# Optimization experiments

Hardware: AMD Instinct MI355X
Metric: run time of the kernel (lower is better)

The kernel has to match this reference:

```python
import jax, jax.numpy as jnp
import numpy as np

N = 100000      # nodes
D = 128         # per-component feature dim
E = 3200000     # edges (avg degree 32)
NUM_CLS = 40
EPS = 1e-7


def lorentz_logmap0(x):
    # Lorentz model, curvature -1, origin o = (1, 0, ..., 0).
    # log_o(x) = arccosh(x0) * (x - x0*o) / ||x - x0*o||  ; keeps full dim, time comp -> 0
    x0 = x[..., :1]
    u = jnp.concatenate([jnp.zeros_like(x0), x[..., 1:]], axis=-1)
    un = jnp.sqrt(jnp.clip(x0 * x0 - 1.0, EPS))
    return jnp.arccosh(jnp.maximum(x0, 1.0)) * u / un


def sphere_logmap0(x):
    # Unit sphere, origin o = (1, 0, ..., 0).
    # log_o(x) = arccos(<o,x>) * (x - <o,x> o) / ||x - <o,x> o||
    c = x[..., :1]
    u = jnp.concatenate([jnp.zeros_like(c), x[..., 1:]], axis=-1)
    un = jnp.sqrt(jnp.clip(1.0 - c * c, EPS))
    return jnp.arccos(jnp.clip(c, -1.0, 1.0)) * u / un


def setup_inputs() -> dict:
    key = jax.random.key(0)
    k1, k2, k3, k4, k5 = jax.random.split(key, 5)
    x_E = jax.random.normal(k1, (N, D), jnp.float32)
    # valid hyperboloid points: x0 = sqrt(1 + ||rest||^2)
    rest = 0.5 * jax.random.normal(k2, (N, D - 1), jnp.float32)
    x0 = jnp.sqrt(1.0 + jnp.sum(rest * rest, axis=-1, keepdims=True))
    x_H = jnp.concatenate([x0, rest], axis=-1)
    # valid sphere points: unit norm
    xs = jax.random.normal(k3, (N, D), jnp.float32)
    x_S = xs / jnp.linalg.norm(xs, axis=-1, keepdims=True)
    W = jax.random.normal(k4, (3 * D, NUM_CLS), jnp.float32) / np.sqrt(3 * D)
    edge_index = jax.random.randint(k5, (2, E), 0, N, dtype=jnp.int32)
    return {"x_E": x_E, "x_H": x_H, "x_S": x_S, "W": W, "edge_index": edge_index}


def reference(x_E, x_H, x_S, W, edge_index):
    # logmap0 projections + concat
    x = jnp.concatenate([x_E, lorentz_logmap0(x_H), sphere_logmap0(x_S)], axis=-1)  # [N, 3D]
    # GCNConv(bias=False): transform first (num_cls << in_dim), then normalized aggregation
    h = x @ W  # [N, C]
    row, col = edge_index[0], edge_index[1]
    loop = jnp.arange(N, dtype=edge_index.dtype)
    row = jnp.concatenate([row, loop])
    col = jnp.concatenate([col, loop])
    deg = jax.ops.segment_sum(jnp.ones_like(col, dtype=h.dtype), col, num_segments=N)
    dinv = jnp.where(deg > 0, jax.lax.rsqrt(jnp.maximum(deg, 1.0)), 0.0)
    norm = dinv[row] * dinv[col]  # [E+N]
    out = jax.ops.segment_sum(h[row] * norm[:, None], col, num_segments=N)  # [N, C]
    return out
```

## Files before the change

### kernel.cpp

```cpp
#include <hip/hip_runtime.h>
#include <math.h>

constexpr int NN   = 100000;
constexpr int DIM  = 128;
constexpr int NE   = 3200000;
constexpr int NCLS = 40;
constexpr float EPSF = 1e-7f;

constexpr int BSH  = 9;
constexpr int BSZ  = 1 << BSH;
constexpr int NBKT = (NN + BSZ - 1) >> BSH;
constexpr int CAP  = 18432;
constexpr int AEPB = 8192;
constexpr int ABLK = (NE + AEPB - 1) / AEPB;

constexpr int GSTR = 64;

typedef __attribute__((ext_vector_type(8))) short bf16x8;
typedef __attribute__((ext_vector_type(8))) unsigned short u16x8;
typedef __attribute__((ext_vector_type(4))) float f32x4;

__device__ __forceinline__ unsigned short f2bf(float f) {
    unsigned u = __builtin_bit_cast(unsigned, f);
    unsigned r = u + 0x7FFFu + ((u >> 16) & 1u);
    return (unsigned short)(r >> 16);
}
__device__ __forceinline__ float bf2f(unsigned short b) {
    return __builtin_bit_cast(float, (unsigned)b << 16);
}

__global__ __launch_bounds__(256) void binA_kernel(const int* __restrict__ row,
                                                   const int* __restrict__ col,
                                                   int* __restrict__ gcur,
                                                   unsigned* __restrict__ pairs) {
    __shared__ int hist[256];
    __shared__ int lofx[256];
    __shared__ int gbase[256];
    __shared__ unsigned sortedw[AEPB];
    __shared__ int dstg[AEPB];

    int t = threadIdx.x;
    int e0 = blockIdx.x * AEPB;
    int cnt = min(AEPB, NE - e0);

    hist[t] = 0;
    __syncthreads();
    for (int k = t; k < cnt; k += 256) atomicAdd(&hist[col[e0 + k] >> BSH], 1);
    __syncthreads();

    int h = hist[t];
    if (t < NBKT && h > 0) gbase[t] = atomicAdd(&gcur[t], h);
    lofx[t] = h;
    __syncthreads();
    for (int d = 1; d < 256; d <<= 1) {
        int o = (t >= d) ? lofx[t - d] : 0;
        __syncthreads();
        lofx[t] += o;
        __syncthreads();
    }
    int excl = lofx[t] - h;
    lofx[t] = excl;
    hist[t] = excl;
    __syncthreads();

    for (int k = t; k < cnt; k += 256) {
        int c = col[e0 + k], r = row[e0 + k];
        int b = c >> BSH;
        int pos = atomicAdd(&hist[b], 1);
        sortedw[pos] = ((unsigned)(c & (BSZ - 1)) << 17) | (unsigned)r;
        dstg[pos] = b * CAP + gbase[b] + (pos - lofx[b]);
    }
    __syncthreads();
    for (int k = t; k < cnt; k += 256) pairs[dstg[k]] = sortedw[k];
}

__global__ __launch_bounds__(1024) void dinv_kernel(const int* __restrict__ gcur,
                                                    const unsigned* __restrict__ pairs,
                                                    float* __restrict__ dinvt) {
    __shared__ int hist[BSZ];
    int t = threadIdx.x;
    int b = blockIdx.x;
    if (t < BSZ) hist[t] = 0;
    __syncthreads();
    int cnt = gcur[b];
    const unsigned* pb = pairs + (size_t)b * CAP;
    for (int i = t; i < cnt; i += 1024) atomicAdd(&hist[pb[i] >> 17], 1);
    __syncthreads();
    if (t < BSZ) {
        int n = (b << BSH) + t;
        if (n < NN) dinvt[n] = rsqrtf((float)(hist[t] + 1));
    }
}

__global__ __launch_bounds__(256) void wpack_kernel(const float* __restrict__ W,
                                                    unsigned short* __restrict__ wbf) {
    int idx = blockIdx.x * 256 + threadIdx.x;
    if (idx >= 12 * 3 * 2 * 64 * 8) return;
    int j    = idx & 7;
    int lane = (idx >> 3) & 63;
    int hl   = (idx >> 9) & 1;
    int rest = idx >> 10;
    int t    = rest % 3;
    int kc   = rest / 3;
    int k = kc * 32 + 8 * (lane >> 4) + j;
    int c = 16 * t + (lane & 15);
    float w = (c < NCLS) ? W[k * NCLS + c] : 0.f;
    unsigned short hi = f2bf(w);
    wbf[idx] = (hl == 0) ? hi : f2bf(w - bf2f(hi));
}

__global__ __launch_bounds__(256) void h_kernel(
    const float* __restrict__ xE, const float* __restrict__ xH,
    const float* __restrict__ xS, const unsigned short* __restrict__ wbf,
    const float* __restrict__ dinvt, unsigned short* __restrict__ gbf) {

    int t = threadIdx.x;
    int lane = t & 63;
    int wv = t >> 6;
    int n0 = blockIdx.x * 64;
    int r  = lane & 15;
    int kq = lane >> 4;
    int myrow = n0 + 16 * wv + r;
    bool rowok = myrow < NN;

    f32x4 acc0 = {0.f, 0.f, 0.f, 0.f};
    f32x4 acc1 = acc0, acc2 = acc0;

    const bf16x8* wfr = reinterpret_cast<const bf16x8*>(wbf);

    for (int m = 0; m < 3; ++m) {
        const float* xb = (m == 0) ? xE : (m == 1) ? xH : xS;
        const float* xrow = xb + (size_t)myrow * DIM;

        float4 xf[8];
#pragma unroll
        for (int kc4 = 0; kc4 < 4; ++kc4) {
            int off = kc4 * 32 + kq * 8;
            xf[2 * kc4]     = rowok ? *reinterpret_cast<const float4*>(xrow + off)
                                    : make_float4(0.f, 0.f, 0.f, 0.f);
            xf[2 * kc4 + 1] = rowok ? *reinterpret_cast<const float4*>(xrow + off + 4)
                                    : make_float4(0.f, 0.f, 0.f, 0.f);
        }

        float scm = 1.f;
        if (m > 0) {
            float x0 = rowok ? xrow[0] : 1.f;
            if (m == 1) {
                scm = acoshf(fmaxf(x0, 1.f)) * rsqrtf(fmaxf(x0 * x0 - 1.f, EPSF));
            } else {
                float cc = fminf(fmaxf(x0, -1.f), 1.f);
                scm = acosf(cc) * rsqrtf(fmaxf(1.f - x0 * x0, EPSF));
            }
        }

#pragma unroll
        for (int kc4 = 0; kc4 < 4; ++kc4) {
            float4 f0 = xf[2 * kc4], f1 = xf[2 * kc4 + 1];
            float a[8] = {f0.x, f0.y, f0.z, f0.w, f1.x, f1.y, f1.z, f1.w};
            if (m > 0 && kc4 == 0 && kq == 0) a[0] = 0.f;

            bf16x8 ah;
#pragma unroll
            for (int j = 0; j < 8; ++j)
                ah[j] = (short)f2bf(a[j] * scm);

            int kc = m * 4 + kc4;
            const bf16x8* wb = wfr + (size_t)(kc * 3) * 2 * 64;
            bf16x8 bh0 = wb[0 * 128 + 0 * 64 + lane];
            bf16x8 bl0 = wb[0 * 128 + 1 * 64 + lane];
            bf16x8 bh1 = wb[1 * 128 + 0 * 64 + lane];
            bf16x8 bl1 = wb[1 * 128 + 1 * 64 + lane];
            bf16x8 bh2 = wb[2 * 128 + 0 * 64 + lane];
            bf16x8 bl2 = wb[2 * 128 + 1 * 64 + lane];

            acc0 = __builtin_amdgcn_mfma_f32_16x16x32_bf16(ah, bh0, acc0, 0, 0, 0);
            acc0 = __builtin_amdgcn_mfma_f32_16x16x32_bf16(ah, bl0, acc0, 0, 0, 0);
            acc1 = __builtin_amdgcn_mfma_f32_16x16x32_bf16(ah, bh1, acc1, 0, 0, 0);
            acc1 = __builtin_amdgcn_mfma_f32_16x16x32_bf16(ah, bl1, acc1, 0, 0, 0);
            acc2 = __builtin_amdgcn_mfma_f32_16x16x32_bf16(ah, bh2, acc2, 0, 0, 0);
            acc2 = __builtin_amdgcn_mfma_f32_16x16x32_bf16(ah, bl2, acc2, 0, 0, 0);
        }
    }

    int nbase = n0 + 16 * wv + 4 * kq;
    float4 dv = make_float4(0.f, 0.f, 0.f, 0.f);
    if (nbase < NN)
        dv = *reinterpret_cast<const float4*>(dinvt + nbase);
    float dg[4] = {dv.x, dv.y, dv.z, dv.w};

#pragma unroll
    for (int i = 0; i < 4; ++i) {
        int n = nbase + i;
        if (n < NN) {
            float di = dg[i];
            unsigned short* gr = gbf + (size_t)n * GSTR;
            gr[r]      = f2bf(acc0[i] * di);
            gr[16 + r] = f2bf(acc1[i] * di);
            if (r < 8)
                gr[32 + r] = f2bf(acc2[i] * di);
        }
    }
}

__global__ __launch_bounds__(1024) void fusedBG_kernel(
    const int* __restrict__ gcur, const unsigned* __restrict__ pairs,
    const unsigned short* __restrict__ gbf, float* __restrict__ out) {

    __shared__ int srow[CAP];
    __shared__ int hist[512];
    __shared__ int sc[1024];

    int t = threadIdx.x;
    int b = blockIdx.x;
    int cnt = gcur[b];
    const unsigned* pb = pairs + (size_t)b * CAP;

    if (t < 512) hist[t] = 0;
    __syncthreads();
    for (int i = t; i < cnt; i += 1024) atomicAdd(&hist[pb[i] >> 17], 1);
    __syncthreads();

    int v = (t < 512) ? hist[t] : 0;
    sc[t] = v;
    __syncthreads();
    for (int d = 1; d < 1024; d <<= 1) {
        int o = (t >= d) ? sc[t - d] : 0;
        __syncthreads();
        sc[t] += o;
        __syncthreads();
    }
    int excl = sc[t] - v;
    __syncthreads();
    if (t < 512) { sc[t] = excl; hist[t] = excl; }
    __syncthreads();

    for (int i = t; i < cnt; i += 1024) {
        unsigned w = pb[i];
        int pos = atomicAdd(&hist[w >> 17], 1);
        srow[pos] = (int)(w & 0x1FFFFu);
    }
    __syncthreads();

    const u16x8* gball = reinterpret_cast<const u16x8*>(gbf);
    for (int task = t; task < BSZ * 5; task += 1024) {
        int c  = task / 5;
        int c8 = task - c * 5;
        int n = (b << BSH) + c;
        if (n >= NN) continue;
        int s = sc[c];
        int e = (c == BSZ - 1) ? cnt : sc[c + 1];
        float dinv = rsqrtf((float)(e - s + 1));

        const u16x8* gb = gball + c8;
        u16x8 sv = gb[(size_t)n * 8];
        float a0[8], a1[8], a2[8], a3[8];
#pragma unroll
        for (int k = 0; k < 8; ++k) {
            a0[k] = bf2f(sv[k]); a1[k] = 0.f; a2[k] = 0.f; a3[k] = 0.f;
        }

        int j = s;
        for (; j + 3 < e; j += 4) {
            int r0 = srow[j], r1 = srow[j + 1], r2 = srow[j + 2], r3 = srow[j + 3];
            u16x8 v0 = gb[(size_t)r0 * 8];
            u16x8 v1 = gb[(size_t)r1 * 8];
            u16x8 v2 = gb[(size_t)r2 * 8];
            u16x8 v3 = gb[(size_t)r3 * 8];
#pragma unroll
            for (int k = 0; k < 8; ++k) {
                a0[k] += bf2f(v0[k]); a1[k] += bf2f(v1[k]);
                a2[k] += bf2f(v2[k]); a3[k] += bf2f(v3[k]);
            }
        }
        for (; j < e; ++j) {
            u16x8 vv = gb[(size_t)srow[j] * 8];
#pragma unroll
            for (int k = 0; k < 8; ++k) a0[k] += bf2f(vv[k]);
        }

        float* on = out + (size_t)n * NCLS + c8 * 8;
        float4 o0, o1;
        o0.x = (a0[0] + a1[0] + a2[0] + a3[0]) * dinv;
        o0.y = (a0[1] + a1[1] + a2[1] + a3[1]) * dinv;
        o0.z = (a0[2] + a1[2] + a2[2] + a3[2]) * dinv;
        o0.w = (a0[3] + a1[3] + a2[3] + a3[3]) * dinv;
        o1.x = (a0[4] + a1[4] + a2[4] + a3[4]) * dinv;
        o1.y = (a0[5] + a1[5] + a2[5] + a3[5]) * dinv;
        o1.z = (a0[6] + a1[6] + a2[6] + a3[6]) * dinv;
        o1.w = (a0[7] + a1[7] + a2[7] + a3[7]) * dinv;
        *reinterpret_cast<float4*>(on)     = o0;
        *reinterpret_cast<float4*>(on + 4) = o1;
    }
}

extern "C" void kernel_launch(void* const* d_in, const int* in_sizes, int n_in,
                              void* d_out, int out_size, void* d_ws, size_t ws_size,
                              hipStream_t stream) {
    const float* xE = (const float*)d_in[0];
    const float* xH = (const float*)d_in[1];
    const float* xS = (const float*)d_in[2];
    const float* W  = (const float*)d_in[3];
    const int*   ei = (const int*)d_in[4];
    const int* row = ei;
    const int* col = ei + NE;
    float* out = (float*)d_out;

    auto pad = [](size_t x) { return (x + 255) & ~(size_t)255; };
    char* p = (char*)d_ws;
    int* gcur = (int*)p;                p += pad((size_t)NBKT * 4);
    unsigned* pairs = (unsigned*)p;     p += pad((size_t)NBKT * CAP * 4);
    unsigned short* gbf = (unsigned short*)p;
    p += pad((size_t)NN * GSTR * 2);
    float* dinvt = (float*)p;           p += pad((size_t)NN * 4);
    unsigned short* wbf = (unsigned short*)p;

    hipMemsetAsync(gcur, 0, (size_t)NBKT * 4, stream);

    wpack_kernel<<<(12 * 3 * 2 * 64 * 8 + 255) / 256, 256, 0, stream>>>(W, wbf);
    binA_kernel<<<ABLK, 256, 0, stream>>>(row, col, gcur, pairs);
    dinv_kernel<<<NBKT, 1024, 0, stream>>>(gcur, pairs, dinvt);
    h_kernel<<<(NN + 63) / 64, 256, 0, stream>>>(xE, xH, xS, wbf, dinvt, gbf);
    fusedBG_kernel<<<NBKT, 1024, 0, stream>>>(gcur, pairs, gbf, out);
}
```

Before: 143.9 us.

## Co-schedule edge binning and dense transform in one interleaved hybrid kernel

Merges the edge-binning kernel and the feature-transform (MFMA) kernel into a single launch where every third block bins edges and the other blocks compute unscaled h rows, so the memory-bound scatter and compute-bound GEMM can overlap on the GPU. The edges-per-bin-block count is halved so the block counts interleave. The dinv scaling moves into the degree kernel, which now rescales the bf16 h rows in place after computing degrees. The cost is an extra read-modify-write pass over gbf and a second bf16 rounding of h.

```diff
diff --git a/kernel.cpp b/kernel.cpp
--- a/kernel.cpp
+++ b/kernel.cpp
@@ -11,8 +11,9 @@
 constexpr int BSZ  = 1 << BSH;
 constexpr int NBKT = (NN + BSZ - 1) >> BSH;
 constexpr int CAP  = 18432;
-constexpr int AEPB = 8192;
+constexpr int AEPB = 4096;
 constexpr int ABLK = (NE + AEPB - 1) / AEPB;
+constexpr int HBLK = (NN + 63) / 64 + 1;
 
 constexpr int GSTR = 64;
 
@@ -29,54 +30,145 @@
     return __builtin_bit_cast(float, (unsigned)b << 16);
 }
 
-__global__ __launch_bounds__(256) void binA_kernel(const int* __restrict__ row,
-                                                   const int* __restrict__ col,
-                                                   int* __restrict__ gcur,
-                                                   unsigned* __restrict__ pairs) {
+__global__ __launch_bounds__(256) void hybrid_kernel(
+    const int* __restrict__ row, const int* __restrict__ col,
+    int* __restrict__ gcur, unsigned* __restrict__ pairs,
+    const float* __restrict__ xE, const float* __restrict__ xH,
+    const float* __restrict__ xS, const unsigned short* __restrict__ wbf,
+    unsigned short* __restrict__ gbf) {
+
     __shared__ int hist[256];
     __shared__ int lofx[256];
     __shared__ int gbase[256];
     __shared__ unsigned sortedw[AEPB];
     __shared__ int dstg[AEPB];
 
+    int bid = blockIdx.x;
     int t = threadIdx.x;
-    int e0 = blockIdx.x * AEPB;
-    int cnt = min(AEPB, NE - e0);
-
-    hist[t] = 0;
-    __syncthreads();
-    for (int k = t; k < cnt; k += 256) atomicAdd(&hist[col[e0 + k] >> BSH], 1);
-    __syncthreads();
-
-    int h = hist[t];
-    if (t < NBKT && h > 0) gbase[t] = atomicAdd(&gcur[t], h);
-    lofx[t] = h;
-    __syncthreads();
-    for (int d = 1; d < 256; d <<= 1) {
-        int o = (t >= d) ? lofx[t - d] : 0;
-        __syncthreads();
-        lofx[t] += o;
-        __syncthreads();
-    }
-    int excl = lofx[t] - h;
-    lofx[t] = excl;
-    hist[t] = excl;
-    __syncthreads();
-
-    for (int k = t; k < cnt; k += 256) {
-        int c = col[e0 + k], r = row[e0 + k];
-        int b = c >> BSH;
-        int pos = atomicAdd(&hist[b], 1);
-        sortedw[pos] = ((unsigned)(c & (BSZ - 1)) << 17) | (unsigned)r;
-        dstg[pos] = b * CAP + gbase[b] + (pos - lofx[b]);
-    }
-    __syncthreads();
-    for (int k = t; k < cnt; k += 256) pairs[dstg[k]] = sortedw[k];
-}
-
-__global__ __launch_bounds__(1024) void dinv_kernel(const int* __restrict__ gcur,
-                                                    const unsigned* __restrict__ pairs,
-                                                    float* __restrict__ dinvt) {
+
+    if (bid % 3 == 0) {
+        int e0 = (bid / 3) * AEPB;
+        int cnt = min(AEPB, NE - e0);
+
+        hist[t] = 0;
+        __syncthreads();
+        for (int k = t; k < cnt; k += 256) atomicAdd(&hist[col[e0 + k] >> BSH], 1);
+        __syncthreads();
+
+        int h = hist[t];
+        if (t < NBKT && h > 0) gbase[t] = atomicAdd(&gcur[t], h);
+        lofx[t] = h;
+        __syncthreads();
+        for (int d = 1; d < 256; d <<= 1) {
+            int o = (t >= d) ? lofx[t - d] : 0;
+            __syncthreads();
+            lofx[t] += o;
+            __syncthreads();
+        }
+        int excl = lofx[t] - h;
+        lofx[t] = excl;
+        hist[t] = excl;
+        __syncthreads();
+
+        for (int k = t; k < cnt; k += 256) {
+            int c = col[e0 + k], r = row[e0 + k];
+            int b = c >> BSH;
+            int pos = atomicAdd(&hist[b], 1);
+            sortedw[pos] = ((unsigned)(c & (BSZ - 1)) << 17) | (unsigned)r;
+            dstg[pos] = b * CAP + gbase[b] + (pos - lofx[b]);
+        }
+        __syncthreads();
+        for (int k = t; k < cnt; k += 256) pairs[dstg[k]] = sortedw[k];
+        return;
+    }
+
+    int hidx = 2 * (bid / 3) + (bid % 3) - 1;
+    int n0 = hidx * 64;
+    if (n0 >= NN) return;
+
+    int lane = t & 63;
+    int wv = t >> 6;
+    int r  = lane & 15;
+    int kq = lane >> 4;
+    int myrow = n0 + 16 * wv + r;
+    bool rowok = myrow < NN;
+
+    f32x4 acc0 = {0.f, 0.f, 0.f, 0.f};
+    f32x4 acc1 = acc0, acc2 = acc0;
+
+    const bf16x8* wfr = reinterpret_cast<const bf16x8*>(wbf);
+
+    for (int m = 0; m < 3; ++m) {
+        const float* xb = (m == 0) ? xE : (m == 1) ? xH : xS;
+        const float* xrow = xb + (size_t)myrow * DIM;
+
+        float4 xf[8];
+#pragma unroll
+        for (int kc4 = 0; kc4 < 4; ++kc4) {
+            int off = kc4 * 32 + kq * 8;
+            xf[2 * kc4]     = rowok ? *reinterpret_cast<const float4*>(xrow + off)
+                                    : make_float4(0.f, 0.f, 0.f, 0.f);
+            xf[2 * kc4 + 1] = rowok ? *reinterpret_cast<const float4*>(xrow + off + 4)
+                                    : make_float4(0.f, 0.f, 0.f, 0.f);
+        }
+
+        float scm = 1.f;
+        if (m > 0) {
+            float x0 = rowok ? xrow[0] : 1.f;
+            if (m == 1) {
+                scm = acoshf(fmaxf(x0, 1.f)) * rsqrtf(fmaxf(x0 * x0 - 1.f, EPSF));
+            } else {
+                float cc = fminf(fmaxf(x0, -1.f), 1.f);
+                scm = acosf(cc) * rsqrtf(fmaxf(1.f - x0 * x0, EPSF));
+            }
+        }
+
+#pragma unroll
+        for (int kc4 = 0; kc4 < 4; ++kc4) {
+            float4 f0 = xf[2 * kc4], f1 = xf[2 * kc4 + 1];
+            float a[8] = {f0.x, f0.y, f0.z, f0.w, f1.x, f1.y, f1.z, f1.w};
+            if (m > 0 && kc4 == 0 && kq == 0) a[0] = 0.f;
+
+            bf16x8 ah;
+#pragma unroll
+            for (int j = 0; j < 8; ++j)
+                ah[j] = (short)f2bf(a[j] * scm);
+
+            int kc = m * 4 + kc4;
+            const bf16x8* wb = wfr + (size_t)(kc * 3) * 2 * 64;
+            bf16x8 bh0 = wb[0 * 128 + 0 * 64 + lane];
+            bf16x8 bl0 = wb[0 * 128 + 1 * 64 + lane];
+            bf16x8 bh1 = wb[1 * 128 + 0 * 64 + lane];
+            bf16x8 bl1 = wb[1 * 128 + 1 * 64 + lane];
+            bf16x8 bh2 = wb[2 * 128 + 0 * 64 + lane];
+            bf16x8 bl2 = wb[2 * 128 + 1 * 64 + lane];
+
+            acc0 = __builtin_amdgcn_mfma_f32_16x16x32_bf16(ah, bh0, acc0, 0, 0, 0);
+            acc0 = __builtin_amdgcn_mfma_f32_16x16x32_bf16(ah, bl0, acc0, 0, 0, 0);
+            acc1 = __builtin_amdgcn_mfma_f32_16x16x32_bf16(ah, bh1, acc1, 0, 0, 0);
+            acc1 = __builtin_amdgcn_mfma_f32_16x16x32_bf16(ah, bl1, acc1, 0, 0, 0);
+            acc2 = __builtin_amdgcn_mfma_f32_16x16x32_bf16(ah, bh2, acc2, 0, 0, 0);
+            acc2 = __builtin_amdgcn_mfma_f32_16x16x32_bf16(ah, bl2, acc2, 0, 0, 0);
+        }
+    }
+
+    int nbase = n0 + 16 * wv + 4 * kq;
+#pragma unroll
+    for (int i = 0; i < 4; ++i) {
+        int n = nbase + i;
+        if (n < NN) {
+            unsigned short* gr = gbf + (size_t)n * GSTR;
+            gr[r]      = f2bf(acc0[i]);
+            gr[16 + r] = f2bf(acc1[i]);
+            if (r < 8)
+                gr[32 + r] = f2bf(acc2[i]);
+        }
+    }
+}
+
+__global__ __launch_bounds__(1024) void dinvscale_kernel(
+    const int* __restrict__ gcur, const unsigned* __restrict__ pairs,
+    unsigned short* __restrict__ gbf) {
     __shared__ int hist[BSZ];
     int t = threadIdx.x;
     int b = blockIdx.x;
@@ -86,9 +178,18 @@
     const unsigned* pb = pairs + (size_t)b * CAP;
     for (int i = t; i < cnt; i += 1024) atomicAdd(&hist[pb[i] >> 17], 1);
     __syncthreads();
-    if (t < BSZ) {
-        int n = (b << BSH) + t;
-        if (n < NN) dinvt[n] = rsqrtf((float)(hist[t] + 1));
+
+    for (int task = t; task < BSZ * 5; task += 1024) {
+        int c = task / 5;
+        int q = task - c * 5;
+        int n = (b << BSH) + c;
+        if (n >= NN) continue;
+        float di = rsqrtf((float)(hist[c] + 1));
+        u16x8* gp = reinterpret_cast<u16x8*>(gbf + (size_t)n * GSTR) + q;
+        u16x8 v = *gp;
+#pragma unroll
+        for (int k = 0; k < 8; ++k) v[k] = (short)f2bf(bf2f(v[k]) * di);
+        *gp = v;
     }
 }
 
@@ -109,99 +210,6 @@
     wbf[idx] = (hl == 0) ? hi : f2bf(w - bf2f(hi));
 }
 
-__global__ __launch_bounds__(256) void h_kernel(
-    const float* __restrict__ xE, const float* __restrict__ xH,
-    const float* __restrict__ xS, const unsigned short* __restrict__ wbf,
-    const float* __restrict__ dinvt, unsigned short* __restrict__ gbf) {
-
-    int t = threadIdx.x;
-    int lane = t & 63;
-    int wv = t >> 6;
-    int n0 = blockIdx.x * 64;
-    int r  = lane & 15;
-    int kq = lane >> 4;
-    int myrow = n0 + 16 * wv + r;
-    bool rowok = myrow < NN;
-
-    f32x4 acc0 = {0.f, 0.f, 0.f, 0.f};
-    f32x4 acc1 = acc0, acc2 = acc0;
-
-    const bf16x8* wfr = reinterpret_cast<const bf16x8*>(wbf);
-
-    for (int m = 0; m < 3; ++m) {
-        const float* xb = (m == 0) ? xE : (m == 1) ? xH : xS;
-        const float* xrow = xb + (size_t)myrow * DIM;
-
-        float4 xf[8];
-#pragma unroll
-        for (int kc4 = 0; kc4 < 4; ++kc4) {
-            int off = kc4 * 32 + kq * 8;
-            xf[2 * kc4]     = rowok ? *reinterpret_cast<const float4*>(xrow + off)
-                                    : make_float4(0.f, 0.f, 0.f, 0.f);
-            xf[2 * kc4 + 1] = rowok ? *reinterpret_cast<const float4*>(xrow + off + 4)
-                                    : make_float4(0.f, 0.f, 0.f, 0.f);
-        }
-
-        float scm = 1.f;
-        if (m > 0) {
-            float x0 = rowok ? xrow[0] : 1.f;
-            if (m == 1) {
-                scm = acoshf(fmaxf(x0, 1.f)) * rsqrtf(fmaxf(x0 * x0 - 1.f, EPSF));
-            } else {
-                float cc = fminf(fmaxf(x0, -1.f), 1.f);
-                scm = acosf(cc) * rsqrtf(fmaxf(1.f - x0 * x0, EPSF));
-            }
-        }
-
-#pragma unroll
-        for (int kc4 = 0; kc4 < 4; ++kc4) {
-            float4 f0 = xf[2 * kc4], f1 = xf[2 * kc4 + 1];
-            float a[8] = {f0.x, f0.y, f0.z, f0.w, f1.x, f1.y, f1.z, f1.w};
-            if (m > 0 && kc4 == 0 && kq == 0) a[0] = 0.f;
-
-            bf16x8 ah;
-#pragma unroll
-            for (int j = 0; j < 8; ++j)
-                ah[j] = (short)f2bf(a[j] * scm);
-
-            int kc = m * 4 + kc4;
-            const bf16x8* wb = wfr + (size_t)(kc * 3) * 2 * 64;
-            bf16x8 bh0 = wb[0 * 128 + 0 * 64 + lane];
-            bf16x8 bl0 = wb[0 * 128 + 1 * 64 + lane];
-            bf16x8 bh1 = wb[1 * 128 + 0 * 64 + lane];
-            bf16x8 bl1 = wb[1 * 128 + 1 * 64 + lane];
-            bf16x8 bh2 = wb[2 * 128 + 0 * 64 + lane];
-            bf16x8 bl2 = wb[2 * 128 + 1 * 64 + lane];
-
-            acc0 = __builtin_amdgcn_mfma_f32_16x16x32_bf16(ah, bh0, acc0, 0, 0, 0);
-            acc0 = __builtin_amdgcn_mfma_f32_16x16x32_bf16(ah, bl0, acc0, 0, 0, 0);
-            acc1 = __builtin_amdgcn_mfma_f32_16x16x32_bf16(ah, bh1, acc1, 0, 0, 0);
-            acc1 = __builtin_amdgcn_mfma_f32_16x16x32_bf16(ah, bl1, acc1, 0, 0, 0);
-            acc2 = __builtin_amdgcn_mfma_f32_16x16x32_bf16(ah, bh2, acc2, 0, 0, 0);
-            acc2 = __builtin_amdgcn_mfma_f32_16x16x32_bf16(ah, bl2, acc2, 0, 0, 0);
-        }
-    }
-
-    int nbase = n0 + 16 * wv + 4 * kq;
-    float4 dv = make_float4(0.f, 0.f, 0.f, 0.f);
-    if (nbase < NN)
-        dv = *reinterpret_cast<const float4*>(dinvt + nbase);
-    float dg[4] = {dv.x, dv.y, dv.z, dv.w};
-
-#pragma unroll
-    for (int i = 0; i < 4; ++i) {
-        int n = nbase + i;
-        if (n < NN) {
-            float di = dg[i];
-            unsigned short* gr = gbf + (size_t)n * GSTR;
-            gr[r]      = f2bf(acc0[i] * di);
-            gr[16 + r] = f2bf(acc1[i] * di);
-            if (r < 8)
-                gr[32 + r] = f2bf(acc2[i] * di);
-        }
-    }
-}
-
 __global__ __launch_bounds__(1024) void fusedBG_kernel(
     const int* __restrict__ gcur, const unsigned* __restrict__ pairs,
     const unsigned short* __restrict__ gbf, float* __restrict__ out) {
@@ -311,14 +319,13 @@
     unsigned* pairs = (unsigned*)p;     p += pad((size_t)NBKT * CAP * 4);
     unsigned short* gbf = (unsigned short*)p;
     p += pad((size_t)NN * GSTR * 2);
-    float* dinvt = (float*)p;           p += pad((size_t)NN * 4);
     unsigned short* wbf = (unsigned short*)p;
 
     hipMemsetAsync(gcur, 0, (size_t)NBKT * 4, stream);
 
     wpack_kernel<<<(12 * 3 * 2 * 64 * 8 + 255) / 256, 256, 0, stream>>>(W, wbf);
-    binA_kernel<<<ABLK, 256, 0, stream>>>(row, col, gcur, pairs);
-    dinv_kernel<<<NBKT, 1024, 0, stream>>>(gcur, pairs, dinvt);
-    h_kernel<<<(NN + 63) / 64, 256, 0, stream>>>(xE, xH, xS, wbf, dinvt, gbf);
+    hybrid_kernel<<<ABLK * 3, 256, 0, stream>>>(row, col, gcur, pairs,
+                                                xE, xH, xS, wbf, gbf);
+    dinvscale_kernel<<<NBKT, 1024, 0, stream>>>(gcur, pairs, gbf);
     fusedBG_kernel<<<NBKT, 1024, 0, stream>>>(gcur, pairs, gbf, out);
 }
```

Result: faster. 130.6 us (-9.3%).
